# Kernel optimization log

Measured on AMD Instinct MI355X. Metric: run time of the kernel, lower is better.

Reference implementation:

```python
import jax, jax.numpy as jnp
import numpy as np

SLOPE = 0.1  # LeakyReLU negative slope

def _inv_sqrt(v):
    # pow(v, -0.5) with inf -> 0 (matches torch isinf masking)
    return jnp.where(v > 0, v ** -0.5, 0.0)

def setup_inputs() -> dict:
    key = jax.random.key(0)
    ks = jax.random.split(key, 5)
    P, D, I, H, R = 2048, 4096, 512, 256, 5
    return {
        "p_feat": jax.random.normal(ks[0], (P, I), dtype=jnp.float32),
        "d_feat": jax.random.normal(ks[1], (D, I), dtype=jnp.float32),
        "p": jnp.arange(P, dtype=jnp.int64),
        "d": jnp.arange(D, dtype=jnp.int64),
        "support": jax.random.uniform(ks[2], (R, P, D), dtype=jnp.float32),
        "p_weight": jax.random.normal(ks[3], (R, I, H), dtype=jnp.float32) * (6.0 / (I + H)) ** 0.5,
        "p_bias": jax.random.normal(ks[4], (H,), dtype=jnp.float32),
    }

def reference(p_feat, d_feat, p, d, support, p_weight, p_bias):
    # dropout p=0.0 -> identity (eval semantics)
    # cumulative weight sum across relations: w_cum[r] = sum_{r'<=r} p_weight[r']
    w_cum = jnp.cumsum(p_weight, axis=0)                 # [R, I, H]
    tmp_p = jnp.einsum('pi,rih->rph', p_feat, w_cum)     # [R, P, H]
    tmp_d = jnp.einsum('di,rih->rdh', d_feat, w_cum)     # [R, D, H]

    # normalize(S) = diag(colsum(S)^-1/2) @ S @ diag(rowsum_axis0(S)^-1/2)
    # (torch code builds NxN diags + matmuls; equivalent to broadcast scaling)
    col_scale = _inv_sqrt(support.sum(axis=1))           # [R, D] (sum over P)
    row_scale = _inv_sqrt(support.sum(axis=2))           # [R, P] (sum over D)
    norm = support * row_scale[:, :, None] * col_scale[:, None, :]  # [R, P, D]
    # note: normalize(S.T) == normalize(S).T, so reuse norm for the drug side

    z_p = jnp.einsum('rpd,rdh->ph', norm[:, p, :], tmp_d)   # gather protein rows
    z_d = jnp.einsum('rpd,rph->dh', norm[:, :, d], tmp_p)   # gather drug rows of S.T
    z_p = z_p + p_bias
    z_d = z_d + p_bias  # d_bias is tied to p_bias

    leaky = lambda x: jnp.where(x >= 0, x, SLOPE * x)
    return (leaky(z_p), leaky(z_d))
```

## Files before the change

### kernel.cpp

```cpp
#include <hip/hip_runtime.h>

typedef __bf16 bf16x8 __attribute__((ext_vector_type(8)));
typedef __bf16 bf16x4 __attribute__((ext_vector_type(4)));
typedef float  f32x4  __attribute__((ext_vector_type(4)));

#define P_  2048
#define D_  4096
#define IC_ 512
#define H_  256
#define R_  5
#define KP_ (R_*D_)
#define KD_ (R_*P_)

__device__ __forceinline__ int swzf(int row){ return ((row>>1) ^ (row>>3)) & 3; }

__device__ __forceinline__ bf16x8 cvt8(float4 a, float4 b){
  bf16x8 o;
  o[0]=(__bf16)a.x; o[1]=(__bf16)a.y; o[2]=(__bf16)a.z; o[3]=(__bf16)a.w;
  o[4]=(__bf16)b.x; o[5]=(__bf16)b.y; o[6]=(__bf16)b.z; o[7]=(__bf16)b.w;
  return o;
}

__device__ __forceinline__ void gl_lds16(const __bf16* g, __bf16* l){
  __builtin_amdgcn_global_load_lds(
    (const __attribute__((address_space(1))) unsigned int*)(g),
    (__attribute__((address_space(3))) unsigned int*)(l), 16, 0, 0);
}

__global__ void k_wcum(const float* __restrict__ pw, __bf16* __restrict__ wct){
  const int h  = threadIdx.x;
  const int i0 = blockIdx.x * 8;
  float acc[8];
  #pragma unroll
  for (int j=0;j<8;++j) acc[j]=0.f;
  for (int r=0;r<R_;++r){
    bf16x8 o;
    #pragma unroll
    for (int j=0;j<8;++j){
      acc[j] += pw[((size_t)r*IC_ + i0 + j)*H_ + h];
      o[j] = (__bf16)acc[j];
    }
    *reinterpret_cast<bf16x8*>(wct + ((size_t)r*H_ + h)*IC_ + i0) = o;
  }
}

__global__ __launch_bounds__(256) void k_prepcs(const float* __restrict__ S,
    __bf16* __restrict__ Sbf, float* __restrict__ rs, float* __restrict__ cspart){
  __shared__ float wsum[32][4];
  const int t = threadIdx.x, lane = t & 63, w = t >> 6;
  const int slab = blockIdx.x;
  const int r = slab >> 6, z = slab & 63;
  const size_t row0 = (size_t)r*P_ + (size_t)z*32;
  const float4* src = reinterpret_cast<const float4*>(S + row0*D_);
  __bf16* dst = Sbf + row0*D_;
  f32x4 ca[4];
  #pragma unroll
  for (int c=0;c<4;++c){ ca[c][0]=0.f; ca[c][1]=0.f; ca[c][2]=0.f; ca[c][3]=0.f; }
  for (int pp=0; pp<32; ++pp){
    float4 v[4];
    #pragma unroll
    for (int c=0;c<4;++c) v[c] = src[(size_t)pp*(D_/4) + t + 256*c];
    float rsum = 0.f;
    #pragma unroll
    for (int c=0;c<4;++c){
      ca[c][0]+=v[c].x; ca[c][1]+=v[c].y; ca[c][2]+=v[c].z; ca[c][3]+=v[c].w;
      rsum += v[c].x+v[c].y+v[c].z+v[c].w;
      bf16x4 o; o[0]=(__bf16)v[c].x; o[1]=(__bf16)v[c].y; o[2]=(__bf16)v[c].z; o[3]=(__bf16)v[c].w;
      *reinterpret_cast<bf16x4*>(dst + (size_t)pp*D_ + (t + 256*c)*4) = o;
    }
    #pragma unroll
    for (int off = 32; off; off >>= 1) rsum += __shfl_xor(rsum, off);
    if (lane == 0) wsum[pp][w] = rsum;
  }
  __syncthreads();
  if (t < 32){
    float s = wsum[t][0]+wsum[t][1]+wsum[t][2]+wsum[t][3];
    rs[row0 + t] = (s > 0.f) ? rsqrtf(s) : 0.f;
  }
  float* o = cspart + ((size_t)z*R_ + r)*D_;
  #pragma unroll
  for (int c=0;c<4;++c) *reinterpret_cast<f32x4*>(o + (t + 256*c)*4) = ca[c];
}

__global__ void k_csfin(const float* __restrict__ cspart, float* __restrict__ cs){
  const int i = blockIdx.x*256 + threadIdx.x;
  float s = 0.f;
  #pragma unroll
  for (int z = 0; z < 64; ++z) s += cspart[(size_t)z*(R_*D_) + i];
  cs[i] = (s > 0.f) ? rsqrtf(s) : 0.f;
}

__global__ __launch_bounds__(256) void k_tmp(const float* __restrict__ p_feat,
    const float* __restrict__ d_feat, const float* __restrict__ rs,
    const float* __restrict__ cs, const __bf16* __restrict__ wct,
    __bf16* __restrict__ Tpt, __bf16* __restrict__ Tdt){
  __shared__ __bf16 As[64*40];
  const int t = threadIdx.x, lane = t & 63, w = t >> 6;
  const int mt = blockIdx.x, r = blockIdx.y;
  const bool isp = mt < (P_/64);
  const float* feat  = isp ? p_feat : d_feat;
  const float* scale = isp ? rs : cs;
  __bf16* outT = isp ? Tpt : Tdt;
  const int M  = isp ? P_ : D_;
  const int RM = isp ? KD_ : KP_;
  const int m0 = (isp ? mt : mt - P_/64)*64;
  const int srow = t >> 2, skc = (t & 3)*8;
  f32x4 acc[4][4];
  #pragma unroll
  for (int a=0;a<4;++a)
    #pragma unroll
    for (int b=0;b<4;++b){ acc[a][b][0]=0.f; acc[a][b][1]=0.f; acc[a][b][2]=0.f; acc[a][b][3]=0.f; }

  for (int ks = 0; ks < IC_; ks += 32){
    __syncthreads();
    {
      const float* g = feat + (size_t)(m0+srow)*IC_ + ks + skc;
      float4 a = *(const float4*)g, b = *(const float4*)(g+4);
      *reinterpret_cast<bf16x8*>(&As[srow*40 + skc]) = cvt8(a,b);
    }
    __syncthreads();
    bf16x8 af[4], bfv[4];
    #pragma unroll
    for (int tt=0;tt<4;++tt)
      af[tt] = *reinterpret_cast<const bf16x8*>(&As[(16*tt + (lane&15))*40 + (lane>>4)*8]);
    #pragma unroll
    for (int cc=0;cc<4;++cc)
      bfv[cc] = *reinterpret_cast<const bf16x8*>(wct + ((size_t)r*H_ + w*64 + 16*cc + (lane&15))*IC_ + ks + (lane>>4)*8);
    #pragma unroll
    for (int tt=0;tt<4;++tt)
      #pragma unroll
      for (int cc=0;cc<4;++cc)
        acc[tt][cc] = __builtin_amdgcn_mfma_f32_16x16x32_bf16(af[tt], bfv[cc], acc[tt][cc], 0, 0, 0);
  }
  #pragma unroll
  for (int tt=0;tt<4;++tt){
    const int mb = m0 + 16*tt + ((lane>>4)<<2);
    const float s0 = scale[r*M+mb+0], s1 = scale[r*M+mb+1],
                s2 = scale[r*M+mb+2], s3 = scale[r*M+mb+3];
    #pragma unroll
    for (int cc=0;cc<4;++cc){
      const int hc = (w<<6) + 16*cc + (lane&15);
      bf16x4 v;
      v[0]=(__bf16)(acc[tt][cc][0]*s0); v[1]=(__bf16)(acc[tt][cc][1]*s1);
      v[2]=(__bf16)(acc[tt][cc][2]*s2); v[3]=(__bf16)(acc[tt][cc][3]*s3);
      *reinterpret_cast<bf16x4*>(outT + (size_t)hc*RM + r*M + mb) = v;
    }
  }
}

__global__ __launch_bounds__(512, 4) void k_z(const __bf16* __restrict__ Sbf,
    const float* __restrict__ rs, const float* __restrict__ cs,
    const __bf16* __restrict__ Tdt, const __bf16* __restrict__ Tpt,
    float* __restrict__ partP, float* __restrict__ partD){
  __shared__ __bf16 As[128*32];
  __shared__ __bf16 Bs[256*32];
  const int t = threadIdx.x, lane = t & 63, w = t >> 6;
  const int wm = w >> 2, wn = w & 3;
  const int bid = blockIdx.x;
  const bool isp = bid < 256;
  const int tile  = isp ? (bid & 15) : ((bid-256) & 31);
  const int split = isp ? (bid >> 4) : ((bid-256) >> 5);
  const int m0 = tile*128;
  const int kbase = split*1280;
  const __bf16* Bsrc = isp ? Tdt : Tpt;
  const int bstr = isp ? KP_ : KD_;
  const int arow  = t >> 2;
  const int aslot = (t & 3) ^ swzf(arow);
  const int prow = t >> 4, d8 = (t & 15)*8;
  const int brow0 = t >> 2, brow1 = 128 + brow0;
  const int bko0 = ((t & 3) ^ swzf(brow0)) * 8;
  const int bko1 = ((t & 3) ^ swzf(brow1)) * 8;
  __bf16* bdst0 = Bs + w*512;
  __bf16* bdst1 = Bs + 4096 + w*512;
  f32x4 acc[4][4];
  #pragma unroll
  for (int a=0;a<4;++a)
    #pragma unroll
    for (int b=0;b<4;++b){ acc[a][b][0]=0.f; acc[a][b][1]=0.f; acc[a][b][2]=0.f; acc[a][b][3]=0.f; }

  for (int ko = 0; ko < 1280; ko += 32){
    const int kg = kbase + ko;
    __syncthreads();
    if (isp){
      const int r = kg >> 12, dd = kg & (D_-1);
      const __bf16* g = Sbf + ((size_t)r*P_ + m0 + arow)*D_ + dd + (t&3)*8;
      const float sc = rs[r*P_ + m0 + arow];
      bf16x8 v = *reinterpret_cast<const bf16x8*>(g);
      bf16x8 o;
      #pragma unroll
      for (int j=0;j<8;++j) o[j] = (__bf16)((float)v[j] * sc);
      *reinterpret_cast<bf16x8*>(&As[arow*32 + aslot*8]) = o;
    } else {
      const int r = kg >> 11, pp = kg & (P_-1);
      const __bf16* g = Sbf + ((size_t)r*P_ + pp + prow)*D_ + m0 + d8;
      bf16x8 v = *reinterpret_cast<const bf16x8*>(g);
      const float4 c1 = *(const float4*)(cs + r*D_ + m0 + d8);
      const float4 c2 = *(const float4*)(cs + r*D_ + m0 + d8 + 4);
      bf16x8 o;
      o[0]=(__bf16)((float)v[0]*c1.x); o[1]=(__bf16)((float)v[1]*c1.y);
      o[2]=(__bf16)((float)v[2]*c1.z); o[3]=(__bf16)((float)v[3]*c1.w);
      o[4]=(__bf16)((float)v[4]*c2.x); o[5]=(__bf16)((float)v[5]*c2.y);
      o[6]=(__bf16)((float)v[6]*c2.z); o[7]=(__bf16)((float)v[7]*c2.w);
      const int kqw = prow >> 3, koff = prow & 7;
      #pragma unroll
      for (int j=0;j<8;++j){
        const int rowd = d8 + j;
        As[rowd*32 + ((kqw ^ swzf(rowd))<<3) + koff] = o[j];
      }
    }
    gl_lds16(Bsrc + (size_t)brow0*bstr + kg + bko0, bdst0);
    gl_lds16(Bsrc + (size_t)brow1*bstr + kg + bko1, bdst1);
    __syncthreads();
    const int kq = lane >> 4;
    bf16x8 bv[4];
    #pragma unroll
    for (int cc=0;cc<4;++cc){
      const int row = wn*64 + 16*cc + (lane&15);
      bv[cc] = *reinterpret_cast<const bf16x8*>(&Bs[row*32 + ((kq ^ swzf(row))<<3)]);
    }
    #pragma unroll
    for (int tt=0;tt<4;++tt){
      const int row = wm*64 + 16*tt + (lane&15);
      bf16x8 af = *reinterpret_cast<const bf16x8*>(&As[row*32 + ((kq ^ swzf(row))<<3)]);
      #pragma unroll
      for (int cc=0;cc<4;++cc)
        acc[tt][cc] = __builtin_amdgcn_mfma_f32_16x16x32_bf16(af, bv[cc], acc[tt][cc], 0, 0, 0);
    }
  }
  float* o = isp ? (partP + (size_t)split*((size_t)P_*H_))
                 : (partD + (size_t)split*((size_t)D_*H_));
  #pragma unroll
  for (int tt=0;tt<4;++tt){
    const int mb = m0 + wm*64 + 16*tt + ((lane>>4)<<2);
    #pragma unroll
    for (int cc=0;cc<4;++cc){
      const int hc = wn*64 + 16*cc + (lane&15);
      #pragma unroll
      for (int j=0;j<4;++j) o[(size_t)(mb+j)*H_ + hc] = acc[tt][cc][j];
    }
  }
}

__global__ void k_reduce(const float* __restrict__ partP, const float* __restrict__ partD,
    const float* __restrict__ bias, float* __restrict__ out){
  const int i = (blockIdx.x*256 + threadIdx.x)*4;
  float4 s; s.x=s.y=s.z=s.w=0.f;
  if (i < P_*H_){
    for (int z = 0; z < 16; ++z){
      float4 v = *(const float4*)(partP + (size_t)z*((size_t)P_*H_) + i);
      s.x+=v.x; s.y+=v.y; s.z+=v.z; s.w+=v.w;
    }
  } else {
    const int j = i - P_*H_;
    for (int z = 0; z < 8; ++z){
      float4 v = *(const float4*)(partD + (size_t)z*((size_t)D_*H_) + j);
      s.x+=v.x; s.y+=v.y; s.z+=v.z; s.w+=v.w;
    }
  }
  const float4 b = *(const float4*)(bias + (i & (H_-1)));
  s.x+=b.x; s.y+=b.y; s.z+=b.z; s.w+=b.w;
  s.x = (s.x>=0.f)? s.x : 0.1f*s.x;
  s.y = (s.y>=0.f)? s.y : 0.1f*s.y;
  s.z = (s.z>=0.f)? s.z : 0.1f*s.z;
  s.w = (s.w>=0.f)? s.w : 0.1f*s.w;
  *(float4*)(out + i) = s;
}

extern "C" void kernel_launch(void* const* d_in, const int* in_sizes, int n_in,
                              void* d_out, int out_size, void* d_ws, size_t ws_size,
                              hipStream_t stream){
  (void)in_sizes; (void)n_in; (void)out_size; (void)ws_size;
  const float* p_feat = (const float*)d_in[0];
  const float* d_feat = (const float*)d_in[1];
  const float* S      = (const float*)d_in[4];
  const float* pw     = (const float*)d_in[5];
  const float* bias   = (const float*)d_in[6];
  float* out = (float*)d_out;

  char* ws = (char*)d_ws;
  __bf16* wct    = (__bf16*)(ws + 0);
  __bf16* Tdt    = (__bf16*)(ws + 1310720);
  __bf16* Tpt    = (__bf16*)(ws + 11796480);
  float*  rs     = (float*) (ws + 17039360);
  float*  cs     = (float*) (ws + 17080320);
  float*  cspart = (float*) (ws + 17162240);
  __bf16* Sbf    = (__bf16*)(ws + 22405120);
  float*  partP  = (float*) (ws + 106291200);
  float*  partD  = (float*) (ws + 139845632);

  k_wcum  <<<64, 256, 0, stream>>>(pw, wct);
  k_prepcs<<<(R_*P_)/32, 256, 0, stream>>>(S, Sbf, rs, cspart);
  k_csfin <<<(R_*D_)/256, 256, 0, stream>>>(cspart, cs);
  k_tmp   <<<dim3((P_+D_)/64, R_), 256, 0, stream>>>(p_feat, d_feat, rs, cs, wct, Tpt, Tdt);
  k_z     <<<512, 512, 0, stream>>>(Sbf, rs, cs, Tdt, Tpt, partP, partD);
  k_reduce<<<((P_+D_)*H_)/1024, 256, 0, stream>>>(partP, partD, bias, out);
}
```

Baseline: 190.7 us.

## Double-buffer LDS in k_z and k_tmp and merge wcum into prep kernel

Adds ping-pong LDS buffers to the main k_z GEMM and the k_tmp projection so the next K-tile's global loads and async LDS copies are issued before the MFMAs on the current tile, with one barrier per iteration instead of two. It also folds the cumulative-weight kernel into the support preprocessing kernel as extra blocks, saving one launch. The cost is doubled LDS use in k_z (48KB), which may lower occupancy at 512 threads, plus extra registers for the prefetched values.

```diff
diff --git a/kernel.cpp b/kernel.cpp
--- a/kernel.cpp
+++ b/kernel.cpp
@@ -27,27 +27,29 @@
     (__attribute__((address_space(3))) unsigned int*)(l), 16, 0, 0);
 }
 
-__global__ void k_wcum(const float* __restrict__ pw, __bf16* __restrict__ wct){
-  const int h  = threadIdx.x;
-  const int i0 = blockIdx.x * 8;
-  float acc[8];
-  #pragma unroll
-  for (int j=0;j<8;++j) acc[j]=0.f;
-  for (int r=0;r<R_;++r){
-    bf16x8 o;
-    #pragma unroll
-    for (int j=0;j<8;++j){
-      acc[j] += pw[((size_t)r*IC_ + i0 + j)*H_ + h];
-      o[j] = (__bf16)acc[j];
-    }
-    *reinterpret_cast<bf16x8*>(wct + ((size_t)r*H_ + h)*IC_ + i0) = o;
-  }
-}
-
-__global__ __launch_bounds__(256) void k_prepcs(const float* __restrict__ S,
-    __bf16* __restrict__ Sbf, float* __restrict__ rs, float* __restrict__ cspart){
+__global__ __launch_bounds__(256) void k_prep2(const float* __restrict__ S,
+    const float* __restrict__ pw, __bf16* __restrict__ Sbf, float* __restrict__ rs,
+    float* __restrict__ cspart, __bf16* __restrict__ wct){
   __shared__ float wsum[32][4];
-  const int t = threadIdx.x, lane = t & 63, w = t >> 6;
+  const int t = threadIdx.x;
+  if (blockIdx.x >= 320){
+    const int h  = t;
+    const int i0 = (blockIdx.x - 320) * 8;
+    float acc[8];
+    #pragma unroll
+    for (int j=0;j<8;++j) acc[j]=0.f;
+    for (int r=0;r<R_;++r){
+      bf16x8 o;
+      #pragma unroll
+      for (int j=0;j<8;++j){
+        acc[j] += pw[((size_t)r*IC_ + i0 + j)*H_ + h];
+        o[j] = (__bf16)acc[j];
+      }
+      *reinterpret_cast<bf16x8*>(wct + ((size_t)r*H_ + h)*IC_ + i0) = o;
+    }
+    return;
+  }
+  const int lane = t & 63, w = t >> 6;
   const int slab = blockIdx.x;
   const int r = slab >> 6, z = slab & 63;
   const size_t row0 = (size_t)r*P_ + (size_t)z*32;
@@ -94,7 +96,7 @@
     const float* __restrict__ d_feat, const float* __restrict__ rs,
     const float* __restrict__ cs, const __bf16* __restrict__ wct,
     __bf16* __restrict__ Tpt, __bf16* __restrict__ Tdt){
-  __shared__ __bf16 As[64*40];
+  __shared__ __bf16 As[2*64*40];
   const int t = threadIdx.x, lane = t & 63, w = t >> 6;
   const int mt = blockIdx.x, r = blockIdx.y;
   const bool isp = mt < (P_/64);
@@ -105,24 +107,31 @@
   const int RM = isp ? KD_ : KP_;
   const int m0 = (isp ? mt : mt - P_/64)*64;
   const int srow = t >> 2, skc = (t & 3)*8;
+  const float* grow = feat + (size_t)(m0+srow)*IC_ + skc;
   f32x4 acc[4][4];
   #pragma unroll
   for (int a=0;a<4;++a)
     #pragma unroll
     for (int b=0;b<4;++b){ acc[a][b][0]=0.f; acc[a][b][1]=0.f; acc[a][b][2]=0.f; acc[a][b][3]=0.f; }
 
+  {
+    float4 a = *(const float4*)grow, b = *(const float4*)(grow+4);
+    *reinterpret_cast<bf16x8*>(&As[srow*40 + skc]) = cvt8(a,b);
+  }
+  __syncthreads();
+  int cur = 0;
   for (int ks = 0; ks < IC_; ks += 32){
-    __syncthreads();
-    {
-      const float* g = feat + (size_t)(m0+srow)*IC_ + ks + skc;
-      float4 a = *(const float4*)g, b = *(const float4*)(g+4);
-      *reinterpret_cast<bf16x8*>(&As[srow*40 + skc]) = cvt8(a,b);
-    }
-    __syncthreads();
+    const bool more = (ks + 32 < IC_);
+    float4 a2, b2;
+    if (more){
+      a2 = *(const float4*)(grow + ks + 32);
+      b2 = *(const float4*)(grow + ks + 36);
+    }
+    const __bf16* Ac = As + cur*2560;
     bf16x8 af[4], bfv[4];
     #pragma unroll
     for (int tt=0;tt<4;++tt)
-      af[tt] = *reinterpret_cast<const bf16x8*>(&As[(16*tt + (lane&15))*40 + (lane>>4)*8]);
+      af[tt] = *reinterpret_cast<const bf16x8*>(&Ac[(16*tt + (lane&15))*40 + (lane>>4)*8]);
     #pragma unroll
     for (int cc=0;cc<4;++cc)
       bfv[cc] = *reinterpret_cast<const bf16x8*>(wct + ((size_t)r*H_ + w*64 + 16*cc + (lane&15))*IC_ + ks + (lane>>4)*8);
@@ -131,6 +140,12 @@
       #pragma unroll
       for (int cc=0;cc<4;++cc)
         acc[tt][cc] = __builtin_amdgcn_mfma_f32_16x16x32_bf16(af[tt], bfv[cc], acc[tt][cc], 0, 0, 0);
+    if (more){
+      __bf16* An = As + (cur^1)*2560;
+      *reinterpret_cast<bf16x8*>(&An[srow*40 + skc]) = cvt8(a2,b2);
+    }
+    __syncthreads();
+    cur ^= 1;
   }
   #pragma unroll
   for (int tt=0;tt<4;++tt){
@@ -152,8 +167,8 @@
     const float* __restrict__ rs, const float* __restrict__ cs,
     const __bf16* __restrict__ Tdt, const __bf16* __restrict__ Tpt,
     float* __restrict__ partP, float* __restrict__ partD){
-  __shared__ __bf16 As[128*32];
-  __shared__ __bf16 Bs[256*32];
+  __shared__ __bf16 As[2*128*32];
+  __shared__ __bf16 Bs[2*256*32];
   const int t = threadIdx.x, lane = t & 63, w = t >> 6;
   const int wm = w >> 2, wn = w & 3;
   const int bid = blockIdx.x;
@@ -167,33 +182,29 @@
   const int arow  = t >> 2;
   const int aslot = (t & 3) ^ swzf(arow);
   const int prow = t >> 4, d8 = (t & 15)*8;
+  const int kqw = prow >> 3, koff = prow & 7;
   const int brow0 = t >> 2, brow1 = 128 + brow0;
   const int bko0 = ((t & 3) ^ swzf(brow0)) * 8;
   const int bko1 = ((t & 3) ^ swzf(brow1)) * 8;
-  __bf16* bdst0 = Bs + w*512;
-  __bf16* bdst1 = Bs + 4096 + w*512;
   f32x4 acc[4][4];
   #pragma unroll
   for (int a=0;a<4;++a)
     #pragma unroll
     for (int b=0;b<4;++b){ acc[a][b][0]=0.f; acc[a][b][1]=0.f; acc[a][b][2]=0.f; acc[a][b][3]=0.f; }
 
-  for (int ko = 0; ko < 1280; ko += 32){
-    const int kg = kbase + ko;
-    __syncthreads();
+  {
+    const int kg = kbase;
     if (isp){
       const int r = kg >> 12, dd = kg & (D_-1);
-      const __bf16* g = Sbf + ((size_t)r*P_ + m0 + arow)*D_ + dd + (t&3)*8;
+      bf16x8 v = *reinterpret_cast<const bf16x8*>(Sbf + ((size_t)r*P_ + m0 + arow)*D_ + dd + (t&3)*8);
       const float sc = rs[r*P_ + m0 + arow];
-      bf16x8 v = *reinterpret_cast<const bf16x8*>(g);
       bf16x8 o;
       #pragma unroll
       for (int j=0;j<8;++j) o[j] = (__bf16)((float)v[j] * sc);
       *reinterpret_cast<bf16x8*>(&As[arow*32 + aslot*8]) = o;
     } else {
       const int r = kg >> 11, pp = kg & (P_-1);
-      const __bf16* g = Sbf + ((size_t)r*P_ + pp + prow)*D_ + m0 + d8;
-      bf16x8 v = *reinterpret_cast<const bf16x8*>(g);
+      bf16x8 v = *reinterpret_cast<const bf16x8*>(Sbf + ((size_t)r*P_ + pp + prow)*D_ + m0 + d8);
       const float4 c1 = *(const float4*)(cs + r*D_ + m0 + d8);
       const float4 c2 = *(const float4*)(cs + r*D_ + m0 + d8 + 4);
       bf16x8 o;
@@ -201,31 +212,76 @@
       o[2]=(__bf16)((float)v[2]*c1.z); o[3]=(__bf16)((float)v[3]*c1.w);
       o[4]=(__bf16)((float)v[4]*c2.x); o[5]=(__bf16)((float)v[5]*c2.y);
       o[6]=(__bf16)((float)v[6]*c2.z); o[7]=(__bf16)((float)v[7]*c2.w);
-      const int kqw = prow >> 3, koff = prow & 7;
       #pragma unroll
       for (int j=0;j<8;++j){
         const int rowd = d8 + j;
         As[rowd*32 + ((kqw ^ swzf(rowd))<<3) + koff] = o[j];
       }
     }
-    gl_lds16(Bsrc + (size_t)brow0*bstr + kg + bko0, bdst0);
-    gl_lds16(Bsrc + (size_t)brow1*bstr + kg + bko1, bdst1);
-    __syncthreads();
+    gl_lds16(Bsrc + (size_t)brow0*bstr + kg + bko0, Bs + w*512);
+    gl_lds16(Bsrc + (size_t)brow1*bstr + kg + bko1, Bs + 4096 + w*512);
+  }
+  __syncthreads();
+
+  int cur = 0;
+  for (int ko = 0; ko < 1280; ko += 32){
+    const bool more = (ko + 32 < 1280);
+    const int nxt = cur ^ 1;
+    bf16x8 va; float sca; float4 c1, c2;
+    if (more){
+      const int kg2 = kbase + ko + 32;
+      if (isp){
+        const int r = kg2 >> 12, dd = kg2 & (D_-1);
+        va = *reinterpret_cast<const bf16x8*>(Sbf + ((size_t)r*P_ + m0 + arow)*D_ + dd + (t&3)*8);
+        sca = rs[r*P_ + m0 + arow];
+      } else {
+        const int r = kg2 >> 11, pp = kg2 & (P_-1);
+        va = *reinterpret_cast<const bf16x8*>(Sbf + ((size_t)r*P_ + pp + prow)*D_ + m0 + d8);
+        c1 = *(const float4*)(cs + r*D_ + m0 + d8);
+        c2 = *(const float4*)(cs + r*D_ + m0 + d8 + 4);
+      }
+      gl_lds16(Bsrc + (size_t)brow0*bstr + kg2 + bko0, Bs + nxt*8192 + w*512);
+      gl_lds16(Bsrc + (size_t)brow1*bstr + kg2 + bko1, Bs + nxt*8192 + 4096 + w*512);
+    }
+    const __bf16* Ac = As + cur*4096;
+    const __bf16* Bc = Bs + cur*8192;
     const int kq = lane >> 4;
     bf16x8 bv[4];
     #pragma unroll
     for (int cc=0;cc<4;++cc){
       const int row = wn*64 + 16*cc + (lane&15);
-      bv[cc] = *reinterpret_cast<const bf16x8*>(&Bs[row*32 + ((kq ^ swzf(row))<<3)]);
+      bv[cc] = *reinterpret_cast<const bf16x8*>(&Bc[row*32 + ((kq ^ swzf(row))<<3)]);
     }
     #pragma unroll
     for (int tt=0;tt<4;++tt){
       const int row = wm*64 + 16*tt + (lane&15);
-      bf16x8 af = *reinterpret_cast<const bf16x8*>(&As[row*32 + ((kq ^ swzf(row))<<3)]);
+      bf16x8 af = *reinterpret_cast<const bf16x8*>(&Ac[row*32 + ((kq ^ swzf(row))<<3)]);
       #pragma unroll
       for (int cc=0;cc<4;++cc)
         acc[tt][cc] = __builtin_amdgcn_mfma_f32_16x16x32_bf16(af, bv[cc], acc[tt][cc], 0, 0, 0);
     }
+    if (more){
+      __bf16* An = As + nxt*4096;
+      if (isp){
+        bf16x8 o;
+        #pragma unroll
+        for (int j=0;j<8;++j) o[j] = (__bf16)((float)va[j] * sca);
+        *reinterpret_cast<bf16x8*>(&An[arow*32 + aslot*8]) = o;
+      } else {
+        bf16x8 o;
+        o[0]=(__bf16)((float)va[0]*c1.x); o[1]=(__bf16)((float)va[1]*c1.y);
+        o[2]=(__bf16)((float)va[2]*c1.z); o[3]=(__bf16)((float)va[3]*c1.w);
+        o[4]=(__bf16)((float)va[4]*c2.x); o[5]=(__bf16)((float)va[5]*c2.y);
+        o[6]=(__bf16)((float)va[6]*c2.z); o[7]=(__bf16)((float)va[7]*c2.w);
+        #pragma unroll
+        for (int j=0;j<8;++j){
+          const int rowd = d8 + j;
+          An[rowd*32 + ((kqw ^ swzf(rowd))<<3) + koff] = o[j];
+        }
+      }
+    }
+    __syncthreads();
+    cur ^= 1;
   }
   float* o = isp ? (partP + (size_t)split*((size_t)P_*H_))
                  : (partD + (size_t)split*((size_t)D_*H_));
@@ -288,8 +344,7 @@
   float*  partP  = (float*) (ws + 106291200);
   float*  partD  = (float*) (ws + 139845632);
 
-  k_wcum  <<<64, 256, 0, stream>>>(pw, wct);
-  k_prepcs<<<(R_*P_)/32, 256, 0, stream>>>(S, Sbf, rs, cspart);
+  k_prep2 <<<384, 256, 0, stream>>>(S, pw, Sbf, rs, cspart, wct);
   k_csfin <<<(R_*D_)/256, 256, 0, stream>>>(cspart, cs);
   k_tmp   <<<dim3((P_+D_)/64, R_), 256, 0, stream>>>(p_feat, d_feat, rs, cs, wct, Tpt, Tdt);
   k_z     <<<512, 512, 0, stream>>>(Sbf, rs, cs, Tdt, Tpt, partP, partD);
```

Result: slower. 203.5 us (+6.7%).

## Move row/col scaling out of GEMM loop into reduce; merge wcum into prep

Applied to the files above, without the earlier changes.

The per-element rs/cs scaling of S tiles inside the z GEMM is removed. The split-K is re-aligned to 1024 so each split stays within one relation, and the per-relation scale is applied to the partial sums in the reduce kernel. This lets the protein-side A tile load go straight to LDS via global_load_lds, with no register round trip. k_wcum is folded into the prep kernel as extra blocks to save a launch. In exchange there are more splits (20/10), which means more partial-sum traffic in the reduce, and the workspace offsets shift.

```diff
diff --git a/kernel.cpp b/kernel.cpp
--- a/kernel.cpp
+++ b/kernel.cpp
@@ -27,27 +27,29 @@
     (__attribute__((address_space(3))) unsigned int*)(l), 16, 0, 0);
 }
 
-__global__ void k_wcum(const float* __restrict__ pw, __bf16* __restrict__ wct){
-  const int h  = threadIdx.x;
-  const int i0 = blockIdx.x * 8;
-  float acc[8];
-  #pragma unroll
-  for (int j=0;j<8;++j) acc[j]=0.f;
-  for (int r=0;r<R_;++r){
-    bf16x8 o;
-    #pragma unroll
-    for (int j=0;j<8;++j){
-      acc[j] += pw[((size_t)r*IC_ + i0 + j)*H_ + h];
-      o[j] = (__bf16)acc[j];
-    }
-    *reinterpret_cast<bf16x8*>(wct + ((size_t)r*H_ + h)*IC_ + i0) = o;
-  }
-}
-
-__global__ __launch_bounds__(256) void k_prepcs(const float* __restrict__ S,
-    __bf16* __restrict__ Sbf, float* __restrict__ rs, float* __restrict__ cspart){
+__global__ __launch_bounds__(256) void k_prep2(const float* __restrict__ S,
+    const float* __restrict__ pw, __bf16* __restrict__ Sbf, float* __restrict__ rs,
+    float* __restrict__ cspart, __bf16* __restrict__ wct){
   __shared__ float wsum[32][4];
-  const int t = threadIdx.x, lane = t & 63, w = t >> 6;
+  const int t = threadIdx.x;
+  if (blockIdx.x >= 320){
+    const int h  = t;
+    const int i0 = (blockIdx.x - 320) * 8;
+    float acc[8];
+    #pragma unroll
+    for (int j=0;j<8;++j) acc[j]=0.f;
+    for (int r=0;r<R_;++r){
+      bf16x8 o;
+      #pragma unroll
+      for (int j=0;j<8;++j){
+        acc[j] += pw[((size_t)r*IC_ + i0 + j)*H_ + h];
+        o[j] = (__bf16)acc[j];
+      }
+      *reinterpret_cast<bf16x8*>(wct + ((size_t)r*H_ + h)*IC_ + i0) = o;
+    }
+    return;
+  }
+  const int lane = t & 63, w = t >> 6;
   const int slab = blockIdx.x;
   const int r = slab >> 6, z = slab & 63;
   const size_t row0 = (size_t)r*P_ + (size_t)z*32;
@@ -149,7 +151,6 @@
 }
 
 __global__ __launch_bounds__(512, 4) void k_z(const __bf16* __restrict__ Sbf,
-    const float* __restrict__ rs, const float* __restrict__ cs,
     const __bf16* __restrict__ Tdt, const __bf16* __restrict__ Tpt,
     float* __restrict__ partP, float* __restrict__ partD){
   __shared__ __bf16 As[128*32];
@@ -157,59 +158,43 @@
   const int t = threadIdx.x, lane = t & 63, w = t >> 6;
   const int wm = w >> 2, wn = w & 3;
   const int bid = blockIdx.x;
-  const bool isp = bid < 256;
-  const int tile  = isp ? (bid & 15) : ((bid-256) & 31);
-  const int split = isp ? (bid >> 4) : ((bid-256) >> 5);
+  const bool isp = bid < 320;
+  const int tile  = isp ? (bid & 15) : ((bid-320) & 31);
+  const int split = isp ? (bid >> 4) : ((bid-320) >> 5);
   const int m0 = tile*128;
-  const int kbase = split*1280;
+  const int kbase = split*1024;
   const __bf16* Bsrc = isp ? Tdt : Tpt;
   const int bstr = isp ? KP_ : KD_;
-  const int arow  = t >> 2;
-  const int aslot = (t & 3) ^ swzf(arow);
+  const int arow = t >> 2;
+  const int akо = ((t & 3) ^ swzf(arow)) * 8;
   const int prow = t >> 4, d8 = (t & 15)*8;
+  const int kqw = prow >> 3, koff = prow & 7;
   const int brow0 = t >> 2, brow1 = 128 + brow0;
   const int bko0 = ((t & 3) ^ swzf(brow0)) * 8;
   const int bko1 = ((t & 3) ^ swzf(brow1)) * 8;
-  __bf16* bdst0 = Bs + w*512;
-  __bf16* bdst1 = Bs + 4096 + w*512;
   f32x4 acc[4][4];
   #pragma unroll
   for (int a=0;a<4;++a)
     #pragma unroll
     for (int b=0;b<4;++b){ acc[a][b][0]=0.f; acc[a][b][1]=0.f; acc[a][b][2]=0.f; acc[a][b][3]=0.f; }
 
-  for (int ko = 0; ko < 1280; ko += 32){
+  for (int ko = 0; ko < 1024; ko += 32){
     const int kg = kbase + ko;
     __syncthreads();
     if (isp){
       const int r = kg >> 12, dd = kg & (D_-1);
-      const __bf16* g = Sbf + ((size_t)r*P_ + m0 + arow)*D_ + dd + (t&3)*8;
-      const float sc = rs[r*P_ + m0 + arow];
-      bf16x8 v = *reinterpret_cast<const bf16x8*>(g);
-      bf16x8 o;
-      #pragma unroll
-      for (int j=0;j<8;++j) o[j] = (__bf16)((float)v[j] * sc);
-      *reinterpret_cast<bf16x8*>(&As[arow*32 + aslot*8]) = o;
+      gl_lds16(Sbf + ((size_t)r*P_ + m0 + arow)*D_ + dd + akо, As + w*512);
     } else {
       const int r = kg >> 11, pp = kg & (P_-1);
-      const __bf16* g = Sbf + ((size_t)r*P_ + pp + prow)*D_ + m0 + d8;
-      bf16x8 v = *reinterpret_cast<const bf16x8*>(g);
-      const float4 c1 = *(const float4*)(cs + r*D_ + m0 + d8);
-      const float4 c2 = *(const float4*)(cs + r*D_ + m0 + d8 + 4);
-      bf16x8 o;
-      o[0]=(__bf16)((float)v[0]*c1.x); o[1]=(__bf16)((float)v[1]*c1.y);
-      o[2]=(__bf16)((float)v[2]*c1.z); o[3]=(__bf16)((float)v[3]*c1.w);
-      o[4]=(__bf16)((float)v[4]*c2.x); o[5]=(__bf16)((float)v[5]*c2.y);
-      o[6]=(__bf16)((float)v[6]*c2.z); o[7]=(__bf16)((float)v[7]*c2.w);
-      const int kqw = prow >> 3, koff = prow & 7;
+      bf16x8 va = *reinterpret_cast<const bf16x8*>(Sbf + ((size_t)r*P_ + pp + prow)*D_ + m0 + d8);
       #pragma unroll
       for (int j=0;j<8;++j){
         const int rowd = d8 + j;
-        As[rowd*32 + ((kqw ^ swzf(rowd))<<3) + koff] = o[j];
+        As[rowd*32 + ((kqw ^ swzf(rowd))<<3) + koff] = va[j];
       }
     }
-    gl_lds16(Bsrc + (size_t)brow0*bstr + kg + bko0, bdst0);
-    gl_lds16(Bsrc + (size_t)brow1*bstr + kg + bko1, bdst1);
+    gl_lds16(Bsrc + (size_t)brow0*bstr + kg + bko0, Bs + w*512);
+    gl_lds16(Bsrc + (size_t)brow1*bstr + kg + bko1, Bs + 4096 + w*512);
     __syncthreads();
     const int kq = lane >> 4;
     bf16x8 bv[4];
@@ -242,19 +227,26 @@
 }
 
 __global__ void k_reduce(const float* __restrict__ partP, const float* __restrict__ partD,
+    const float* __restrict__ rs, const float* __restrict__ cs,
     const float* __restrict__ bias, float* __restrict__ out){
   const int i = (blockIdx.x*256 + threadIdx.x)*4;
   float4 s; s.x=s.y=s.z=s.w=0.f;
   if (i < P_*H_){
-    for (int z = 0; z < 16; ++z){
+    const int p = i >> 8;
+    #pragma unroll
+    for (int z = 0; z < 20; ++z){
+      const float sc = rs[(z>>2)*P_ + p];
       float4 v = *(const float4*)(partP + (size_t)z*((size_t)P_*H_) + i);
-      s.x+=v.x; s.y+=v.y; s.z+=v.z; s.w+=v.w;
+      s.x+=sc*v.x; s.y+=sc*v.y; s.z+=sc*v.z; s.w+=sc*v.w;
     }
   } else {
     const int j = i - P_*H_;
-    for (int z = 0; z < 8; ++z){
+    const int d = j >> 8;
+    #pragma unroll
+    for (int z = 0; z < 10; ++z){
+      const float sc = cs[(z>>1)*D_ + d];
       float4 v = *(const float4*)(partD + (size_t)z*((size_t)D_*H_) + j);
-      s.x+=v.x; s.y+=v.y; s.z+=v.z; s.w+=v.w;
+      s.x+=sc*v.x; s.y+=sc*v.y; s.z+=sc*v.z; s.w+=sc*v.w;
     }
   }
   const float4 b = *(const float4*)(bias + (i & (H_-1)));
@@ -286,12 +278,11 @@
   float*  cspart = (float*) (ws + 17162240);
   __bf16* Sbf    = (__bf16*)(ws + 22405120);
   float*  partP  = (float*) (ws + 106291200);
-  float*  partD  = (float*) (ws + 139845632);
-
-  k_wcum  <<<64, 256, 0, stream>>>(pw, wct);
-  k_prepcs<<<(R_*P_)/32, 256, 0, stream>>>(S, Sbf, rs, cspart);
+  float*  partD  = (float*) (ws + 148234240);
+
+  k_prep2 <<<384, 256, 0, stream>>>(S, pw, Sbf, rs, cspart, wct);
   k_csfin <<<(R_*D_)/256, 256, 0, stream>>>(cspart, cs);
   k_tmp   <<<dim3((P_+D_)/64, R_), 256, 0, stream>>>(p_feat, d_feat, rs, cs, wct, Tpt, Tdt);
-  k_z     <<<512, 512, 0, stream>>>(Sbf, rs, cs, Tdt, Tpt, partP, partD);
-  k_reduce<<<((P_+D_)*H_)/1024, 256, 0, stream>>>(partP, partD, bias, out);
-}
+  k_z     <<<640, 512, 0, stream>>>(Sbf, Tdt, Tpt, partP, partD);
+  k_reduce<<<((P_+D_)*H_)/1024, 256, 0, stream>>>(partP, partD, rs, cs, bias, out);
+}
```

New measurement: 211.3 us. 10.8% more time.
